# Performance work log

Hardware: AMD Instinct MI355X
Metric: run time of the kernel (lower is better)

Reference implementation:

```python
import jax, jax.numpy as jnp
import numpy as np


def setup_inputs() -> dict:
    V, D, E = 4096, 128, 12288
    key = jax.random.key(0)
    k1, k2, k3 = jax.random.split(key, 3)
    features = jax.random.normal(k1, (V, D), dtype=jnp.float32)
    # random self-loop-free edge list
    v0 = jax.random.randint(k2, (E,), 0, V)
    off = jax.random.randint(k3, (E,), 1, V)
    v1 = (v0 + off) % V
    edges = jnp.stack([v0, v1]).astype(jnp.int32)  # [2, E]
    # manifold-style neighbor matrix: interior edges share 2 faces
    neighbor = (jnp.zeros((V, V), jnp.int32)
                .at[edges[0], edges[1]].set(2)
                .at[edges[1], edges[0]].set(2))
    return {"features": features, "edges": edges, "neighbor": neighbor}


def _collapse(features, edges, neighbor):
    """Greedy heap-order edge collapse. The heap is built once and only popped,
    so pop order == edges sorted by priority ||f[v0]||^2 + ||f[v1]||^2.
    Returns merge matrix A (f_out = A @ f_in), alive vertex mask, final count."""
    V = neighbor.shape[0]
    target = jnp.int32(V // 2)
    pri = jnp.sum(features * features, axis=1)          # [V]
    epri = pri[edges[0]] + pri[edges[1]]                # [E]
    order = jnp.argsort(epri)                           # heappop order (stable ties)
    alive0 = jnp.ones((V,), bool)
    A0 = jnp.eye(V, dtype=jnp.float32)
    cnt0 = jnp.int32(V)

    def step(carry, e):
        alive, n, A, cnt = carry
        v0 = edges[0, e]
        v1 = edges[1, e]
        do = (cnt > target) & alive[v0] & alive[v1] & (n[v0, v1] == 2)
        # merged neighbor row for v0; v1 dies
        r = (n[v0] + n[v1]).at[v0].set(0).at[v1].set(0)
        row0 = jnp.where(do, r, n[v0])
        row1 = jnp.where(do, jnp.zeros_like(r), n[v1])
        n = (n.at[v0, :].set(row0).at[:, v0].set(row0)
              .at[v1, :].set(row1).at[:, v1].set(row1))
        arow = jnp.where(do, 0.5 * (A[v0] + A[v1]), A[v0])
        A = A.at[v0].set(arow)
        alive = alive.at[v1].set(alive[v1] & jnp.logical_not(do))
        cnt = cnt - do.astype(jnp.int32)
        return (alive, n, A, cnt), None

    (alive, n, A, cnt), _ = jax.lax.scan(step, (alive0, neighbor, A0, cnt0), order)
    return A, alive, cnt


def reference(features, edges, neighbor):
    edges = edges.astype(jnp.int32)
    A, alive, cnt = _collapse(features, edges, neighbor)
    # clean_up() compacts removed vertices; under jit we mask dead rows instead
    pooled = (A @ features) * alive[:, None].astype(features.dtype)
    return pooled, alive, cnt
```

## Files before the change

kernel.cpp:

```cpp
#include <hip/hip_runtime.h>
#include <stdint.h>

#define V 4096
#define D 128
#define E 12288
#define NPAD 16384
#define HALF 8192
#define TARGET 2048
#define MAXM (V - TARGET)
#define ROWU32 256
#define CAP 16

#define WAIT_VM0   0x0F70
#define WAIT_LGKM0 0xC07F

#define WS_N      0u
#define WS_PRI    (V * ROWU32 * 4u)
#define WS_KEYS   (WS_PRI + V * 4u)
#define WS_PK     (WS_KEYS + NPAD * 8u)
#define WS_PAIRS  (WS_PK + E * 4u)
#define WS_MCOUNT (WS_PAIRS + MAXM * 4u)
#define WS_ALIVE  (WS_MCOUNT + 16u)

__device__ __forceinline__ unsigned getf(const uint4& r, int c) {
    unsigned lo = (c & 2) ? r.z : r.x;
    unsigned hi = (c & 2) ? r.w : r.y;
    return (c & 1) ? hi : lo;
}

__global__ void k_scatter(const int* __restrict__ edges, unsigned* __restrict__ n32) {
    int e = blockIdx.x * 256 + threadIdx.x;
    if (e < E) {
        int a = edges[e], b = edges[E + e];
        atomicOr(&n32[a * ROWU32 + (b >> 4)], 2u << ((b & 15) * 2));
        atomicOr(&n32[b * ROWU32 + (a >> 4)], 2u << ((a & 15) * 2));
    }
}

__global__ void k_pri(const float* __restrict__ f, float* __restrict__ pri) {
    int v = blockIdx.x * 256 + threadIdx.x;
    if (v < V) {
        const float* p = f + v * D;
        float r[8];
#pragma unroll
        for (int j = 0; j < 8; j++) r[j] = __fmul_rn(p[j], p[j]);
        for (int i = 8; i < D; i += 8) {
#pragma unroll
            for (int j = 0; j < 8; j++)
                r[j] = __fadd_rn(r[j], __fmul_rn(p[i + j], p[i + j]));
        }
        float s01 = __fadd_rn(r[0], r[1]);
        float s23 = __fadd_rn(r[2], r[3]);
        float s45 = __fadd_rn(r[4], r[5]);
        float s67 = __fadd_rn(r[6], r[7]);
        pri[v] = __fadd_rn(__fadd_rn(s01, s23), __fadd_rn(s45, s67));
    }
}

__global__ void k_keys(const int* __restrict__ edges, const float* __restrict__ pri,
                       unsigned long long* __restrict__ keys) {
    int s = blockIdx.x * 256 + threadIdx.x;
    if (s < NPAD) {
        unsigned long long rec;
        if (s < E) {
            int a = edges[s], b = edges[E + s];
            float k = __fadd_rn(pri[a], pri[b]);
            rec = ((unsigned long long)__float_as_uint(k) << 32) | (unsigned)s;
        } else {
            rec = (0xFFFFFFFFull << 32) | (unsigned)s;
        }
        keys[s] = rec;
    }
}

__launch_bounds__(1024)
__global__ void k_sort2(unsigned long long* __restrict__ keys) {
    __shared__ unsigned long long srt[HALF];
    const int tid = threadIdx.x;
    unsigned long long* base = keys + blockIdx.x * HALF;
    for (int s = tid; s < HALF; s += 1024) srt[s] = base[s];
    __syncthreads();
    for (int k = 2; k <= HALF; k <<= 1) {
        for (int j = k >> 1; j >= 1; j >>= 1) {
            for (int i = tid; i < HALF; i += 1024) {
                int ixj = i ^ j;
                if (ixj > i) {
                    unsigned long long x = srt[i], y = srt[ixj];
                    bool up = ((i & k) == 0);
                    if ((x > y) == up) { srt[i] = y; srt[ixj] = x; }
                }
            }
            __syncthreads();
        }
    }
    for (int s = tid; s < HALF; s += 1024) base[s] = srt[s];
}

__launch_bounds__(64)
__global__ void k_mergepath(const unsigned long long* __restrict__ keys,
                            const int* __restrict__ edges, unsigned* __restrict__ pkG) {
    int t = blockIdx.x * 64 + threadIdx.x;
    if (t >= E / 64) return;
    const unsigned long long* A = keys;
    const unsigned long long* B = keys + HALF;
    int d = t * 64;
    int lo = d > HALF ? d - HALF : 0;
    int hi = d < HALF ? d : HALF;
    while (lo < hi) {
        int mid = (lo + hi) >> 1;
        if (A[mid] < B[d - 1 - mid]) lo = mid + 1; else hi = mid;
    }
    int ia = lo, ib = d - lo;
    for (int o = d; o < d + 64; o++) {
        bool takeA = (ib >= HALF) || (ia < HALF && A[ia] < B[ib]);
        unsigned long long r = takeA ? A[ia++] : B[ib++];
        int e = (int)(r & 0xFFFFFFFFull);
        int a = edges[e], b = edges[E + e];
        pkG[o] = ((unsigned)a << 16) | (unsigned)b;
    }
}

__launch_bounds__(64, 1)
__global__ void k_collapse(const unsigned* __restrict__ pkG, unsigned* n32,
                           unsigned* __restrict__ pairsG, int* __restrict__ mcountG,
                           uint8_t* __restrict__ aliveG, float* __restrict__ out) {
    __shared__ unsigned shPk[64];
    __shared__ unsigned shRR[CAP * ROWU32];
    __shared__ uint8_t alive[V];
    const int lane = threadIdx.x;
    for (int v = lane; v < V; v += 64) alive[v] = 1;
    __builtin_amdgcn_s_waitcnt(WAIT_LGKM0);

    int cnt = V, mcount = 0;
    bool done = false;

    for (int w = 0; w < E && !done; w += 64) {
        __builtin_amdgcn_s_waitcnt(WAIT_VM0);
        unsigned pkv = pkG[w + lane];
        const int a = (int)(pkv >> 16), b = (int)(pkv & 0xFFFFu);
        shPk[lane] = pkv;
        unsigned wv = *(volatile unsigned*)(n32 + a * ROWU32 + (b >> 4));
        unsigned fv = (wv >> ((b & 15) * 2)) & 3u;
        __builtin_amdgcn_s_waitcnt(WAIT_LGKM0);
        bool av = alive[a] && alive[b];
        bool dec = false;

        for (int rnd = 0; rnd < 96 && !done; rnd++) {
            bool flag = !dec && av && (fv == 2u);
            unsigned long long mF = __ballot(flag);
            if (!mF) break;
            int limit = cnt - TARGET; if (limit > CAP) limit = CAP;

            unsigned candPk[CAP]; int candLane[CAP];
            int F = 0;
            unsigned long long mIt = mF;
#pragma unroll
            for (int k = 0; k < CAP; k++) {
                int i = -1; unsigned cp = 0u;
                if (mIt) { i = __ffsll(mIt) - 1; mIt &= mIt - 1ull; F = k + 1; cp = shPk[i]; }
                candLane[k] = i; candPk[k] = cp;
            }
            int cutoff = mIt ? (__ffsll(mIt) - 1) : 64;

            unsigned long long B = 0ull;
            unsigned accBits = 0u; int nacc = 0;
            bool myPois = false; int myK = -1;
#pragma unroll
            for (int k = 0; k < CAP; k++) {
                if (k < F) {
                    int i = candLane[k];
                    if (nacc >= limit) { if (i < cutoff) cutoff = i; }
                    else {
                        int pa = (int)(candPk[k] >> 16), pb = (int)(candPk[k] & 0xFFFFu);
                        unsigned long long bits = (1ull << ((pa ^ (pa >> 6)) & 63)) |
                                                  (1ull << ((pb ^ (pb >> 6)) & 63));
                        bool conf = (B & bits) != 0ull;
                        if (!conf) { accBits |= 1u << k; nacc++; if (lane == i) myK = k; }
                        B |= bits;
                        if (i < lane && (pa == a || pa == b || pb == a || pb == b))
                            myPois = true;
                    }
                }
            }
            if (!dec && !flag && !myPois && lane < cutoff) dec = true;

            __builtin_amdgcn_s_waitcnt(WAIT_VM0);
            uint4 RA[CAP], RB[CAP];
#pragma unroll
            for (int k = 0; k < CAP; k++) {
                if ((accBits >> k) & 1u) {
                    int v0 = (int)(candPk[k] >> 16), v1 = (int)(candPk[k] & 0xFFFFu);
                    RA[k] = *((const uint4*)(n32 + v0 * ROWU32) + lane);
                    RB[k] = *((const uint4*)(n32 + v1 * ROWU32) + lane);
                }
            }

            unsigned keptBits = 0u;
            uint4 RBU = make_uint4(0u, 0u, 0u, 0u);
            uint4 MV0 = make_uint4(0u, 0u, 0u, 0u);
#pragma unroll
            for (int k = 0; k < CAP; k++) {
                if ((accBits >> k) & 1u) {
                    int v0 = (int)(candPk[k] >> 16), v1 = (int)(candPk[k] & 0xFFFFu);
                    bool c = false;
                    if ((v0 >> 6) == lane)
                        c |= ((getf(RBU, (v0 >> 4) & 3) >> ((v0 & 15) * 2)) & 3u) != 0u;
                    if ((v1 >> 6) == lane)
                        c |= ((getf(RBU, (v1 >> 4) & 3) >> ((v1 & 15) * 2)) & 3u) != 0u;
                    c |= ((RB[k].x & MV0.x) | (RB[k].y & MV0.y) |
                          (RB[k].z & MV0.z) | (RB[k].w & MV0.w)) != 0u;
                    if (__ballot(c) == 0ull) {
                        keptBits |= 1u << k;
                        RBU.x |= RB[k].x; RBU.y |= RB[k].y;
                        RBU.z |= RB[k].z; RBU.w |= RB[k].w;
                        if ((v0 >> 6) == lane) {
                            int c4 = (v0 >> 4) & 3; unsigned bit = 3u << ((v0 & 15) * 2);
                            if (c4 == 0) MV0.x |= bit; else if (c4 == 1) MV0.y |= bit;
                            else if (c4 == 2) MV0.z |= bit; else MV0.w |= bit;
                        }
                    }
                }
            }
            if (myK >= 0 && ((keptBits >> myK) & 1u)) dec = true;

#pragma unroll
            for (int k = 0; k < CAP; k++) {
                if ((keptBits >> k) & 1u) {
                    int v0 = (int)(candPk[k] >> 16), v1 = (int)(candPk[k] & 0xFFFFu);
                    uint4 ra = RA[k], rb = RB[k];
                    uint4 rr;
                    rr.x = ra.x | rb.x | ((ra.x & rb.x & 0xAAAAAAAAu) >> 1);
                    rr.y = ra.y | rb.y | ((ra.y & rb.y & 0xAAAAAAAAu) >> 1);
                    rr.z = ra.z | rb.z | ((ra.z & rb.z & 0xAAAAAAAAu) >> 1);
                    rr.w = ra.w | rb.w | ((ra.w & rb.w & 0xAAAAAAAAu) >> 1);
                    if ((v0 >> 6) == lane) {
                        int c4 = (v0 >> 4) & 3; unsigned m = ~(3u << ((v0 & 15) * 2));
                        if (c4 == 0) rr.x &= m; else if (c4 == 1) rr.y &= m;
                        else if (c4 == 2) rr.z &= m; else rr.w &= m;
                    }
                    if ((v1 >> 6) == lane) {
                        int c4 = (v1 >> 4) & 3; unsigned m = ~(3u << ((v1 & 15) * 2));
                        if (c4 == 0) rr.x &= m; else if (c4 == 1) rr.y &= m;
                        else if (c4 == 2) rr.z &= m; else rr.w &= m;
                    }
                    *((uint4*)(n32 + v0 * ROWU32) + lane) = rr;
                    *((uint4*)(shRR + k * ROWU32) + lane) = rr;
                    int sh0 = (v0 & 15) * 2, wi0 = v0 >> 4;
#pragma unroll
                    for (int c = 0; c < 4; c++) {
                        unsigned bb = getf(rb, c);
                        if (!bb) continue;
                        unsigned aa = getf(ra, c), vv = getf(rr, c);
                        int xbase = (lane << 6) + (c << 4);
                        unsigned t = bb;
                        while (t) {
                            int q = (__ffs(t) - 1) >> 1;
                            t &= ~(3u << (q * 2));
                            int x = xbase + q;
                            if (x != v0 && x != v1) {
                                unsigned dx = (((aa >> (q * 2)) ^ (vv >> (q * 2))) & 3u) << sh0;
                                if (dx) atomicXor(n32 + x * ROWU32 + wi0, dx);
                            }
                        }
                    }
                    if (lane == 0) {
                        alive[v1] = 0;
                        pairsG[mcount] = ((unsigned)v0 << 16) | (unsigned)v1;
                    }
                    mcount++; cnt--;
                }
            }
            __builtin_amdgcn_s_waitcnt(WAIT_LGKM0);

            int ja = -1, jb = -1;
#pragma unroll
            for (int k = 0; k < CAP; k++) {
                if ((keptBits >> k) & 1u) {
                    int v0 = (int)(candPk[k] >> 16), v1 = (int)(candPk[k] & 0xFFFFu);
                    if (a == v1 || b == v1) dec = true;
                    if (a == v0) ja = k;
                    if (b == v0) jb = k;
                }
            }
            if (jb >= 0)      fv = (shRR[jb * ROWU32 + (a >> 4)] >> ((a & 15) * 2)) & 3u;
            else if (ja >= 0) fv = (shRR[ja * ROWU32 + (b >> 4)] >> ((b & 15) * 2)) & 3u;

            if (cnt == TARGET) done = true;
        }
    }

    for (int v = lane; v < V; v += 64) {
        uint8_t ao = alive[v];
        aliveG[v] = ao;
        out[V * D + v] = ao ? 1.0f : 0.0f;
    }
    if (lane == 0) { mcountG[0] = mcount; out[V * D + V] = (float)cnt; }
}

__launch_bounds__(256)
__global__ void k_apply(const float* __restrict__ f, const unsigned* __restrict__ pairsG,
                        const int* __restrict__ mcountG, float* __restrict__ out) {
    __shared__ unsigned pl[MAXM];
    __shared__ int rootL[256];
    __shared__ float wL[256];
    const int tid = threadIdx.x;
    const int mc = mcountG[0];
    for (int j = tid; j < mc; j += 256) pl[j] = pairsG[j];
    __syncthreads();
    int cur = blockIdx.x * 256 + tid;
    float w = 1.0f;
    for (int j = 0; j < mc; j++) {
        unsigned p = pl[j];
        int v0 = (int)(p >> 16), v1 = (int)(p & 0xFFFFu);
        if (cur == v1) { cur = v0; w *= 0.5f; }
        else if (cur == v0) w *= 0.5f;
    }
    rootL[tid] = cur;
    wL[tid] = w;
    __syncthreads();
    const int sub = tid >> 7;
    const int d = tid & 127;
    for (int s = 0; s < 256; s += 2) {
        int idx = s + sub;
        int vv = blockIdx.x * 256 + idx;
        atomicAdd(&out[rootL[idx] * D + d], wL[idx] * f[vv * D + d]);
    }
}

extern "C" void kernel_launch(void* const* d_in, const int* in_sizes, int n_in,
                              void* d_out, int out_size, void* d_ws, size_t ws_size,
                              hipStream_t stream) {
    (void)in_sizes; (void)n_in; (void)out_size; (void)ws_size;
    const float* features = (const float*)d_in[0];
    const int* edges = (const int*)d_in[1];
    uint8_t* ws = (uint8_t*)d_ws;
    unsigned* n32 = (unsigned*)(ws + WS_N);
    float* pri = (float*)(ws + WS_PRI);
    unsigned long long* keys = (unsigned long long*)(ws + WS_KEYS);
    unsigned* pkG = (unsigned*)(ws + WS_PK);
    unsigned* pairsG = (unsigned*)(ws + WS_PAIRS);
    int* mcountG = (int*)(ws + WS_MCOUNT);
    uint8_t* aliveG = ws + WS_ALIVE;
    float* out = (float*)d_out;

    hipMemsetAsync(n32, 0, (size_t)V * ROWU32 * 4, stream);
    hipMemsetAsync(out, 0, (size_t)V * D * sizeof(float), stream);
    k_pri<<<(V + 255) / 256, 256, 0, stream>>>(features, pri);
    k_scatter<<<(E + 255) / 256, 256, 0, stream>>>(edges, n32);
    k_keys<<<(NPAD + 255) / 256, 256, 0, stream>>>(edges, pri, keys);
    k_sort2<<<2, 1024, 0, stream>>>(keys);
    k_mergepath<<<(E / 64 + 63) / 64, 64, 0, stream>>>(keys, edges, pkG);
    k_collapse<<<1, 64, 0, stream>>>(pkG, n32, pairsG, mcountG, aliveG, out);
    k_apply<<<V / 256, 256, 0, stream>>>(features, pairsG, mcountG, out);
}
```

Baseline: 3.875 ms.

## Stage collapse candidate rows in LDS via global_load_lds and simplify candidate selection

The single-wave collapse loop no longer holds up to 16 row pairs in register arrays. Candidate rows are now copied straight into a shared-memory buffer with global_load_lds and read back from LDS for the conflict check and the merge. Candidate selection switches from fully unrolled loops over cached packed pairs to dynamic bitmask loops that use shuffles, with a 128-bit multiplicative-hash conflict filter and a scan cap. The poison/cutoff early-decision logic is dropped, so undecided lanes just retry in later rounds. The aim is to cut register pressure and unrolled-code overhead in this latency-bound serial loop. The costs are an extra LDS round trip per row and possibly more rounds.

```diff
diff --git a/kernel.cpp b/kernel.cpp
--- a/kernel.cpp
+++ b/kernel.cpp
@@ -10,6 +10,7 @@
 #define MAXM (V - TARGET)
 #define ROWU32 256
 #define CAP 16
+#define SCANCAP 24
 
 #define WAIT_VM0   0x0F70
 #define WAIT_LGKM0 0xC07F
@@ -22,10 +23,21 @@
 #define WS_MCOUNT (WS_PAIRS + MAXM * 4u)
 #define WS_ALIVE  (WS_MCOUNT + 16u)
 
+typedef const __attribute__((address_space(1))) unsigned* gas1_t;
+typedef __attribute__((address_space(3))) unsigned* las3_t;
+
 __device__ __forceinline__ unsigned getf(const uint4& r, int c) {
     unsigned lo = (c & 2) ? r.z : r.x;
     unsigned hi = (c & 2) ? r.w : r.y;
     return (c & 1) ? hi : lo;
+}
+__device__ __forceinline__ void orf(uint4& r, int c, unsigned bits) {
+    if (c == 0) r.x |= bits; else if (c == 1) r.y |= bits;
+    else if (c == 2) r.z |= bits; else r.w |= bits;
+}
+__device__ __forceinline__ void andf(uint4& r, int c, unsigned msk) {
+    if (c == 0) r.x &= msk; else if (c == 1) r.y &= msk;
+    else if (c == 2) r.z &= msk; else r.w &= msk;
 }
 
 __global__ void k_scatter(const int* __restrict__ edges, unsigned* __restrict__ n32) {
@@ -124,8 +136,7 @@
 __global__ void k_collapse(const unsigned* __restrict__ pkG, unsigned* n32,
                            unsigned* __restrict__ pairsG, int* __restrict__ mcountG,
                            uint8_t* __restrict__ aliveG, float* __restrict__ out) {
-    __shared__ unsigned shPk[64];
-    __shared__ unsigned shRR[CAP * ROWU32];
+    __shared__ unsigned shRows[2 * CAP * ROWU32];
     __shared__ uint8_t alive[V];
     const int lane = threadIdx.x;
     for (int v = lane; v < V; v += 64) alive[v] = 1;
@@ -138,153 +149,143 @@
         __builtin_amdgcn_s_waitcnt(WAIT_VM0);
         unsigned pkv = pkG[w + lane];
         const int a = (int)(pkv >> 16), b = (int)(pkv & 0xFFFFu);
-        shPk[lane] = pkv;
         unsigned wv = *(volatile unsigned*)(n32 + a * ROWU32 + (b >> 4));
         unsigned fv = (wv >> ((b & 15) * 2)) & 3u;
-        __builtin_amdgcn_s_waitcnt(WAIT_LGKM0);
-        bool av = alive[a] && alive[b];
-        bool dec = false;
-
-        for (int rnd = 0; rnd < 96 && !done; rnd++) {
-            bool flag = !dec && av && (fv == 2u);
-            unsigned long long mF = __ballot(flag);
+        bool dec = !(alive[a] && alive[b]);
+
+        while (!done) {
+            if (!dec && fv != 2u) dec = true;
+            unsigned long long mF = __ballot(!dec);
             if (!mF) break;
             int limit = cnt - TARGET; if (limit > CAP) limit = CAP;
 
-            unsigned candPk[CAP]; int candLane[CAP];
-            int F = 0;
-            unsigned long long mIt = mF;
-#pragma unroll
-            for (int k = 0; k < CAP; k++) {
-                int i = -1; unsigned cp = 0u;
-                if (mIt) { i = __ffsll(mIt) - 1; mIt &= mIt - 1ull; F = k + 1; cp = shPk[i]; }
-                candLane[k] = i; candPk[k] = cp;
-            }
-            int cutoff = mIt ? (__ffsll(mIt) - 1) : 64;
-
-            unsigned long long B = 0ull;
-            unsigned accBits = 0u; int nacc = 0;
-            bool myPois = false; int myK = -1;
-#pragma unroll
-            for (int k = 0; k < CAP; k++) {
-                if (k < F) {
-                    int i = candLane[k];
-                    if (nacc >= limit) { if (i < cutoff) cutoff = i; }
-                    else {
-                        int pa = (int)(candPk[k] >> 16), pb = (int)(candPk[k] & 0xFFFFu);
-                        unsigned long long bits = (1ull << ((pa ^ (pa >> 6)) & 63)) |
-                                                  (1ull << ((pb ^ (pb >> 6)) & 63));
-                        bool conf = (B & bits) != 0ull;
-                        if (!conf) { accBits |= 1u << k; nacc++; if (lane == i) myK = k; }
-                        B |= bits;
-                        if (i < lane && (pa == a || pa == b || pb == a || pb == b))
-                            myPois = true;
-                    }
-                }
-            }
-            if (!dec && !flag && !myPois && lane < cutoff) dec = true;
+            unsigned long long accLanes = 0ull;
+            unsigned long long B0 = 0ull, B1 = 0ull;
+            int nacc = 0, scanned = 0;
+            {
+                unsigned long long mIt = mF;
+                while (mIt && nacc < limit && scanned < SCANCAP) {
+                    int i = __ffsll(mIt) - 1; mIt &= mIt - 1ull;
+                    int ai = __shfl(a, i), bi = __shfl(b, i);
+                    unsigned ha = ((unsigned)ai * 2654435761u) >> 25;
+                    unsigned hb = ((unsigned)bi * 2654435761u) >> 25;
+                    unsigned long long m0 = 0ull, m1 = 0ull;
+                    if (ha & 64) m1 |= 1ull << (ha & 63); else m0 |= 1ull << (ha & 63);
+                    if (hb & 64) m1 |= 1ull << (hb & 63); else m0 |= 1ull << (hb & 63);
+                    bool conf = ((B0 & m0) | (B1 & m1)) != 0ull;
+                    if (!conf) { accLanes |= 1ull << i; nacc++; }
+                    B0 |= m0; B1 |= m1;
+                    scanned++;
+                }
+            }
 
             __builtin_amdgcn_s_waitcnt(WAIT_VM0);
-            uint4 RA[CAP], RB[CAP];
-#pragma unroll
-            for (int k = 0; k < CAP; k++) {
-                if ((accBits >> k) & 1u) {
-                    int v0 = (int)(candPk[k] >> 16), v1 = (int)(candPk[k] & 0xFFFFu);
-                    RA[k] = *((const uint4*)(n32 + v0 * ROWU32) + lane);
-                    RB[k] = *((const uint4*)(n32 + v1 * ROWU32) + lane);
-                }
-            }
-
-            unsigned keptBits = 0u;
-            uint4 RBU = make_uint4(0u, 0u, 0u, 0u);
-            uint4 MV0 = make_uint4(0u, 0u, 0u, 0u);
-#pragma unroll
-            for (int k = 0; k < CAP; k++) {
-                if ((accBits >> k) & 1u) {
-                    int v0 = (int)(candPk[k] >> 16), v1 = (int)(candPk[k] & 0xFFFFu);
+            {
+                unsigned long long am = accLanes; int k = 0;
+                while (am) {
+                    int i = __ffsll(am) - 1; am &= am - 1ull;
+                    int v0 = __shfl(a, i), v1 = __shfl(b, i);
+                    __builtin_amdgcn_global_load_lds(
+                        (gas1_t)(n32 + v0 * ROWU32 + lane * 4),
+                        (las3_t)(shRows + (2 * k) * ROWU32), 16, 0, 0);
+                    __builtin_amdgcn_global_load_lds(
+                        (gas1_t)(n32 + v1 * ROWU32 + lane * 4),
+                        (las3_t)(shRows + (2 * k + 1) * ROWU32), 16, 0, 0);
+                    k++;
+                }
+            }
+            __builtin_amdgcn_s_waitcnt(WAIT_VM0);
+            __builtin_amdgcn_s_waitcnt(WAIT_LGKM0);
+
+            unsigned long long keptLanes = 0ull;
+            {
+                uint4 RBU = make_uint4(0u, 0u, 0u, 0u);
+                uint4 MV0 = make_uint4(0u, 0u, 0u, 0u);
+                unsigned long long am = accLanes; int k = 0;
+                while (am) {
+                    int i = __ffsll(am) - 1; am &= am - 1ull;
+                    int v0 = __shfl(a, i), v1 = __shfl(b, i);
+                    uint4 rb = *((const uint4*)(shRows + (2 * k + 1) * ROWU32) + lane);
                     bool c = false;
                     if ((v0 >> 6) == lane)
                         c |= ((getf(RBU, (v0 >> 4) & 3) >> ((v0 & 15) * 2)) & 3u) != 0u;
                     if ((v1 >> 6) == lane)
                         c |= ((getf(RBU, (v1 >> 4) & 3) >> ((v1 & 15) * 2)) & 3u) != 0u;
-                    c |= ((RB[k].x & MV0.x) | (RB[k].y & MV0.y) |
-                          (RB[k].z & MV0.z) | (RB[k].w & MV0.w)) != 0u;
+                    c |= ((rb.x & MV0.x) | (rb.y & MV0.y) |
+                          (rb.z & MV0.z) | (rb.w & MV0.w)) != 0u;
                     if (__ballot(c) == 0ull) {
-                        keptBits |= 1u << k;
-                        RBU.x |= RB[k].x; RBU.y |= RB[k].y;
-                        RBU.z |= RB[k].z; RBU.w |= RB[k].w;
-                        if ((v0 >> 6) == lane) {
-                            int c4 = (v0 >> 4) & 3; unsigned bit = 3u << ((v0 & 15) * 2);
-                            if (c4 == 0) MV0.x |= bit; else if (c4 == 1) MV0.y |= bit;
-                            else if (c4 == 2) MV0.z |= bit; else MV0.w |= bit;
-                        }
+                        keptLanes |= 1ull << i;
+                        RBU.x |= rb.x; RBU.y |= rb.y; RBU.z |= rb.z; RBU.w |= rb.w;
+                        if ((v0 >> 6) == lane) orf(MV0, (v0 >> 4) & 3, 3u << ((v0 & 15) * 2));
                     }
-                }
-            }
-            if (myK >= 0 && ((keptBits >> myK) & 1u)) dec = true;
-
+                    k++;
+                }
+            }
+
+            {
+                unsigned long long am = accLanes; int k = 0;
+                while (am) {
+                    int i = __ffsll(am) - 1; am &= am - 1ull;
+                    if ((keptLanes >> i) & 1ull) {
+                        int v0 = __shfl(a, i), v1 = __shfl(b, i);
+                        uint4 ra = *((const uint4*)(shRows + (2 * k) * ROWU32) + lane);
+                        uint4 rb = *((const uint4*)(shRows + (2 * k + 1) * ROWU32) + lane);
+                        uint4 rr;
+                        rr.x = ra.x | rb.x | ((ra.x & rb.x & 0xAAAAAAAAu) >> 1);
+                        rr.y = ra.y | rb.y | ((ra.y & rb.y & 0xAAAAAAAAu) >> 1);
+                        rr.z = ra.z | rb.z | ((ra.z & rb.z & 0xAAAAAAAAu) >> 1);
+                        rr.w = ra.w | rb.w | ((ra.w & rb.w & 0xAAAAAAAAu) >> 1);
+                        if ((v0 >> 6) == lane) andf(rr, (v0 >> 4) & 3, ~(3u << ((v0 & 15) * 2)));
+                        if ((v1 >> 6) == lane) andf(rr, (v1 >> 4) & 3, ~(3u << ((v1 & 15) * 2)));
+                        *((uint4*)(n32 + v0 * ROWU32) + lane) = rr;
+                        *((uint4*)(shRows + (2 * k) * ROWU32) + lane) = rr;
+                        int sh0 = (v0 & 15) * 2, wi0 = v0 >> 4;
 #pragma unroll
-            for (int k = 0; k < CAP; k++) {
-                if ((keptBits >> k) & 1u) {
-                    int v0 = (int)(candPk[k] >> 16), v1 = (int)(candPk[k] & 0xFFFFu);
-                    uint4 ra = RA[k], rb = RB[k];
-                    uint4 rr;
-                    rr.x = ra.x | rb.x | ((ra.x & rb.x & 0xAAAAAAAAu) >> 1);
-                    rr.y = ra.y | rb.y | ((ra.y & rb.y & 0xAAAAAAAAu) >> 1);
-                    rr.z = ra.z | rb.z | ((ra.z & rb.z & 0xAAAAAAAAu) >> 1);
-                    rr.w = ra.w | rb.w | ((ra.w & rb.w & 0xAAAAAAAAu) >> 1);
-                    if ((v0 >> 6) == lane) {
-                        int c4 = (v0 >> 4) & 3; unsigned m = ~(3u << ((v0 & 15) * 2));
-                        if (c4 == 0) rr.x &= m; else if (c4 == 1) rr.y &= m;
-                        else if (c4 == 2) rr.z &= m; else rr.w &= m;
-                    }
-                    if ((v1 >> 6) == lane) {
-                        int c4 = (v1 >> 4) & 3; unsigned m = ~(3u << ((v1 & 15) * 2));
-                        if (c4 == 0) rr.x &= m; else if (c4 == 1) rr.y &= m;
-                        else if (c4 == 2) rr.z &= m; else rr.w &= m;
-                    }
-                    *((uint4*)(n32 + v0 * ROWU32) + lane) = rr;
-                    *((uint4*)(shRR + k * ROWU32) + lane) = rr;
-                    int sh0 = (v0 & 15) * 2, wi0 = v0 >> 4;
-#pragma unroll
-                    for (int c = 0; c < 4; c++) {
-                        unsigned bb = getf(rb, c);
-                        if (!bb) continue;
-                        unsigned aa = getf(ra, c), vv = getf(rr, c);
-                        int xbase = (lane << 6) + (c << 4);
-                        unsigned t = bb;
-                        while (t) {
-                            int q = (__ffs(t) - 1) >> 1;
-                            t &= ~(3u << (q * 2));
-                            int x = xbase + q;
-                            if (x != v0 && x != v1) {
-                                unsigned dx = (((aa >> (q * 2)) ^ (vv >> (q * 2))) & 3u) << sh0;
-                                if (dx) atomicXor(n32 + x * ROWU32 + wi0, dx);
+                        for (int c = 0; c < 4; c++) {
+                            unsigned bb = getf(rb, c);
+                            if (!bb) continue;
+                            unsigned aa = getf(ra, c), vvv = getf(rr, c);
+                            int xbase = (lane << 6) + (c << 4);
+                            unsigned t = bb;
+                            while (t) {
+                                int q = (__ffs(t) - 1) >> 1;
+                                t &= ~(3u << (q * 2));
+                                int x = xbase + q;
+                                if (x != v0 && x != v1) {
+                                    unsigned dx =
+                                        (((aa >> (q * 2)) ^ (vvv >> (q * 2))) & 3u) << sh0;
+                                    if (dx) atomicXor(n32 + x * ROWU32 + wi0, dx);
+                                }
                             }
                         }
+                        if (lane == 0) {
+                            alive[v1] = 0;
+                            pairsG[mcount] = ((unsigned)v0 << 16) | (unsigned)v1;
+                        }
+                        mcount++; cnt--;
                     }
-                    if (lane == 0) {
-                        alive[v1] = 0;
-                        pairsG[mcount] = ((unsigned)v0 << 16) | (unsigned)v1;
+                    k++;
+                }
+            }
+            __builtin_amdgcn_s_waitcnt(WAIT_LGKM0);
+
+            {
+                int slot = -1, fld = 0;
+                unsigned long long am = accLanes; int k = 0;
+                while (am) {
+                    int i = __ffsll(am) - 1; am &= am - 1ull;
+                    if ((keptLanes >> i) & 1ull) {
+                        int v0 = __shfl(a, i), v1 = __shfl(b, i);
+                        if (a == v1 || b == v1) dec = true;
+                        if (lane == i) dec = true;
+                        if (b == v0) { slot = 2 * k; fld = a; }
+                        else if (a == v0) { slot = 2 * k; fld = b; }
                     }
-                    mcount++; cnt--;
-                }
-            }
-            __builtin_amdgcn_s_waitcnt(WAIT_LGKM0);
-
-            int ja = -1, jb = -1;
-#pragma unroll
-            for (int k = 0; k < CAP; k++) {
-                if ((keptBits >> k) & 1u) {
-                    int v0 = (int)(candPk[k] >> 16), v1 = (int)(candPk[k] & 0xFFFFu);
-                    if (a == v1 || b == v1) dec = true;
-                    if (a == v0) ja = k;
-                    if (b == v0) jb = k;
-                }
-            }
-            if (jb >= 0)      fv = (shRR[jb * ROWU32 + (a >> 4)] >> ((a & 15) * 2)) & 3u;
-            else if (ja >= 0) fv = (shRR[ja * ROWU32 + (b >> 4)] >> ((b & 15) * 2)) & 3u;
-
+                    k++;
+                }
+                if (slot >= 0 && !dec)
+                    fv = (shRows[slot * ROWU32 + (fld >> 4)] >> ((fld & 15) * 2)) & 3u;
+            }
             if (cnt == TARGET) done = true;
         }
     }
```

Result: no change. 3.826 ms (-1.3%).
